# Kernel tuning notes

Measured on AMD Instinct MI355X. Metric: run time of the kernel, lower is better.

## Reference

```python
import jax, jax.numpy as jnp
import numpy as np

N_NODES = 50000
N_EDGES = 1600000
NODE_DIM = 128
EDGE_DIM = 64
HIDDEN = 128
K_HOPS = 2  # DGL TAGConv default k=2


def _uniform(key, shape, fan_in):
    bound = 1.0 / np.sqrt(fan_in)
    return jax.random.uniform(key, shape, jnp.float32, -bound, bound)


def setup_inputs() -> dict:
    key = jax.random.key(0)
    ks = jax.random.split(key, 12)
    d_msg_in = NODE_DIM + EDGE_DIM
    d_c1_in = (HIDDEN + NODE_DIM) * (K_HOPS + 1)
    d_c2_in = HIDDEN * (K_HOPS + 1)
    return {
        "node_fea": jax.random.normal(ks[0], (N_NODES, NODE_DIM), jnp.float32),
        "edge_fea": jax.random.normal(ks[1], (N_EDGES, EDGE_DIM), jnp.float32),
        "src": jax.random.randint(ks[2], (N_EDGES,), 0, N_NODES),
        "dst": jax.random.randint(ks[3], (N_EDGES,), 0, N_NODES),
        "msg_W": _uniform(ks[4], (d_msg_in, HIDDEN), d_msg_in),
        "msg_b": _uniform(ks[5], (HIDDEN,), d_msg_in),
        "W1": _uniform(ks[6], (d_c1_in, HIDDEN), d_c1_in),
        "b1": _uniform(ks[7], (HIDDEN,), d_c1_in),
        "W2": _uniform(ks[8], (d_c2_in, HIDDEN), d_c2_in),
        "b2": _uniform(ks[9], (HIDDEN,), d_c2_in),
        "Wp": _uniform(ks[10], (HIDDEN, 1), HIDDEN),
        "bp": _uniform(ks[11], (1,), HIDDEN),
    }


def reference(node_fea, edge_fea, src, dst, msg_W, msg_b, W1, b1, W2, b2, Wp, bp):
    n = node_fea.shape[0]
    # --- edge message: relu(Linear([src_fea, edge_fea])) then scatter-sum to dst ---
    msg = jax.nn.relu(jnp.concatenate([node_fea[src], edge_fea], axis=1) @ msg_W + msg_b)
    h_neigh = jax.ops.segment_sum(msg, dst, num_segments=n)  # [N, H]

    # --- TAGConv (k=2) symmetric in-degree normalization, DGL-style ---
    deg = jax.ops.segment_sum(jnp.ones((dst.shape[0],), node_fea.dtype), dst, num_segments=n)
    norm = jnp.maximum(deg, 1.0) ** -0.5  # [N]

    def prop(x):  # x: [N, D] -> norm * A^T (norm * x)
        return norm[:, None] * jax.ops.segment_sum((x * norm[:, None])[src], dst, num_segments=n)

    def tagconv(x, W, b):
        h1 = prop(x)
        h2 = prop(h1)
        return jnp.concatenate([x, h1, h2], axis=1) @ W + b

    h = jax.nn.relu(tagconv(jnp.concatenate([node_fea, h_neigh], axis=1), W1, b1))
    h = jax.nn.relu(tagconv(h, W2, b2))

    # --- dgl.mean_nodes (single graph) then predict ---
    hg = jnp.mean(h, axis=0)  # [H]
    return hg @ Wp + bp  # [1]
```

## Files before the change

### kernel.cpp

```cpp
#include <hip/hip_runtime.h>
#include <hip/hip_bf16.h>


typedef __attribute__((ext_vector_type(8))) short short8;
typedef __attribute__((ext_vector_type(4))) float f32x4;
typedef __attribute__((ext_vector_type(4))) unsigned u32x4;
typedef unsigned short ushort_t;
typedef unsigned char uchar_t;

static __device__ __forceinline__ unsigned short f2bf(float x) {
  union { float f; unsigned u; } v{x};
  unsigned r = v.u + 0x7FFF + ((v.u >> 16) & 1);
  return (unsigned short)(r >> 16);
}
static __device__ __forceinline__ float bf2f(unsigned short h) {
  union { unsigned u; float f; } v{(unsigned)h << 16};
  return v.f;
}
static __device__ __forceinline__ float u2f(unsigned u) {
  union { unsigned u; float f; } v{u};
  return v.f;
}
static __device__ __forceinline__ unsigned cvtpk(float a, float b) {
  unsigned r;
  asm("v_cvt_pk_bf16_f32 %0, %1, %2" : "=v"(r) : "v"(a), "v"(b));
  return r;
}
static __device__ __forceinline__ uchar_t f2fp8(float x) {
  return (uchar_t)(__builtin_amdgcn_cvt_pk_fp8_f32(x, 0.f, 0, false) & 0xff);
}
static __device__ __forceinline__ ushort_t pk2fp8(float a, float b) {
  return (ushort_t)(__builtin_amdgcn_cvt_pk_fp8_f32(a, b, 0, false) & 0xffff);
}

__global__ void k_deg(const int* __restrict__ dst, int* __restrict__ deg, int E) {
  int i = blockIdx.x * blockDim.x + threadIdx.x;
  int stride = gridDim.x * blockDim.x;
  for (; i < E; i += stride) atomicAdd(&deg[dst[i]], 1);
}

__global__ void k_scan(const int* __restrict__ deg, float* __restrict__ norm,
                       int* __restrict__ offs, int* __restrict__ cursor, int N) {
  __shared__ int part[1024];
  const int t = threadIdx.x;
  const int C = (N + 1023) >> 10;
  const int b = t * C, e = min(b + C, N);
  int s = 0;
  for (int i = b; i < e; ++i) s += deg[i];
  part[t] = s;
  __syncthreads();
  for (int ofs = 1; ofs < 1024; ofs <<= 1) {
    int v = (t >= ofs) ? part[t - ofs] : 0;
    __syncthreads();
    part[t] += v;
    __syncthreads();
  }
  int base = (t == 0) ? 0 : part[t - 1];
  for (int i = b; i < e; ++i) {
    offs[i] = base;
    cursor[i] = base;
    int d = deg[i];
    base += d;
    norm[i] = rsqrtf((float)max(d, 1));
  }
  if (t == 0) offs[N] = part[1023];
}

__global__ void k_csr(const int* __restrict__ src, const int* __restrict__ dst,
                      int* __restrict__ cursor, int* __restrict__ csr_srcnode,
                      int* __restrict__ csr_eid, int* __restrict__ pos2node, int E) {
  int i = blockIdx.x * blockDim.x + threadIdx.x;
  int stride = gridDim.x * blockDim.x;
  for (; i < E; i += stride) {
    int d = dst[i];
    int pos = atomicAdd(&cursor[d], 1);
    csr_srcnode[pos] = src[i];
    csr_eid[pos] = i;
    pos2node[pos] = d;
  }
}

__global__ void k_prepAll(const float* __restrict__ msg_W, const float* __restrict__ W1,
                          const float* __restrict__ W2, ushort_t* __restrict__ WfT_hi,
                          ushort_t* __restrict__ WfT_lo, ushort_t* __restrict__ WfB_hi,
                          ushort_t* __restrict__ WfB_lo, ushort_t* __restrict__ Wf1_hi,
                          ushort_t* __restrict__ Wf1_lo, ushort_t* __restrict__ Wf2_hi,
                          ushort_t* __restrict__ Wf2_lo) {
  int id = blockIdx.x * 256 + threadIdx.x;
  const float* W;
  ushort_t *dh, *dl;
  int lid;
  if (id < 16384) {
    W = msg_W; dh = WfT_hi; dl = WfT_lo; lid = id;
  } else if (id < 24576) {
    W = msg_W + 128 * 128; dh = WfB_hi; dl = WfB_lo; lid = id - 16384;
  } else if (id < 122880) {
    int sub = id - 24576;
    int s = sub >> 15;
    lid = sub & 32767;
    W = W1 + (size_t)s * 256 * 128;
    dh = Wf1_hi + (size_t)s * 32768;
    dl = Wf1_lo + (size_t)s * 32768;
  } else if (id < 172032) {
    int sub = id - 122880;
    int s = sub >> 14;
    lid = sub & 16383;
    W = W2 + (size_t)s * 128 * 128;
    dh = Wf2_hi + (size_t)s * 16384;
    dl = Wf2_lo + (size_t)s * 16384;
  } else {
    return;
  }
  int j = lid & 7;
  int l = (lid >> 3) & 63;
  int rest = lid >> 9;
  int ks = rest & 1, nt = (rest >> 1) & 7, kc = rest >> 4;
  int k = kc * 64 + ks * 32 + (l >> 4) * 8 + j;
  int col = nt * 16 + (l & 15);
  float w = W[(size_t)k * 128 + col];
  unsigned short hi = f2bf(w);
  unsigned short lo = f2bf(w - bf2f(hi));
  dh[lid] = hi;
  dl[lid] = lo;
}

static __device__ __forceinline__ void stage_hi(const float* base, int sq, int sr,
                                                ushort_t* Xh) {
#pragma unroll
  for (int i2 = 0; i2 < 2; ++i2) {
    const int o = sq * 2 + i2;
    f32x4 a4 = *(const f32x4*)(base + sq * 16 + i2 * 8);
    f32x4 b4 = *(const f32x4*)(base + sq * 16 + i2 * 8 + 4);
    u32x4 vh;
    vh[0] = cvtpk(a4[0], a4[1]);
    vh[1] = cvtpk(a4[2], a4[3]);
    vh[2] = cvtpk(b4[0], b4[1]);
    vh[3] = cvtpk(b4[2], b4[3]);
    const int slot = (sr >> 4) * 128 + o * 16 + (sr & 15);
    *(u32x4*)(Xh + (size_t)slot * 8) = vh;
  }
}

__global__ __launch_bounds__(256) void k_mm(
    const float* __restrict__ A0, const ushort_t* __restrict__ Wf_hi,
    const ushort_t* __restrict__ Wf_lo, const float* __restrict__ bias,
    uchar_t* __restrict__ outZ8, int M, int KC) {
  __shared__ __align__(16) char lds[40960];
  ushort_t* Xh = (ushort_t*)lds;
  ushort_t* Whi = (ushort_t*)(lds + 8192);
  ushort_t* Wlo = (ushort_t*)(lds + 24576);

  const int t = threadIdx.x;
  const int m0 = blockIdx.x * 64;
  const int l = t & 63, mt = t >> 6;
  const int sr = t & 63, sq = t >> 6;
  const int row = min(m0 + sr, M - 1);

  f32x4 acc[8];
#pragma unroll
  for (int nt = 0; nt < 8; ++nt) acc[nt] = (f32x4){0.f, 0.f, 0.f, 0.f};

  for (int kc = 0; kc < KC; ++kc) {
    __syncthreads();
    {
      const ulong2* gh = (const ulong2*)(Wf_hi + (size_t)kc * 8192);
      const ulong2* gl = (const ulong2*)(Wf_lo + (size_t)kc * 8192);
#pragma unroll
      for (int i = 0; i < 4; ++i) {
        ((ulong2*)Whi)[i * 256 + t] = gh[i * 256 + t];
        ((ulong2*)Wlo)[i * 256 + t] = gl[i * 256 + t];
      }
    }
    stage_hi(A0 + (size_t)row * 128 + kc * 64, sq, sr, Xh);
    __syncthreads();
    const short8* Xh8 = (const short8*)Xh;
    const short8* Wh8 = (const short8*)Whi;
    const short8* Wl8 = (const short8*)Wlo;
#pragma unroll
    for (int ks = 0; ks < 2; ++ks) {
      short8 ah = Xh8[mt * 128 + ks * 64 + l];
#pragma unroll
      for (int nt = 0; nt < 8; ++nt) {
        short8 bh = Wh8[(nt * 2 + ks) * 64 + l];
        short8 bl = Wl8[(nt * 2 + ks) * 64 + l];
        acc[nt] = __builtin_amdgcn_mfma_f32_16x16x32_bf16(ah, bh, acc[nt], 0, 0, 0);
        acc[nt] = __builtin_amdgcn_mfma_f32_16x16x32_bf16(ah, bl, acc[nt], 0, 0, 0);
      }
    }
  }
  const int l15 = l & 15, lh = l >> 4;
#pragma unroll
  for (int nt = 0; nt < 8; ++nt) {
    const int col = nt * 16 + l15;
#pragma unroll
    for (int rg = 0; rg < 4; ++rg) {
      const int r = m0 + mt * 16 + lh * 4 + rg;
      if (r < M) outZ8[(size_t)r * 128 + col] = f2fp8(acc[nt][rg] + bias[col]);
    }
  }
}

template <int BF16A>
__global__ __launch_bounds__(256) void k_mm3(
    const void* __restrict__ A0v, const float* __restrict__ A1, int split64,
    const ushort_t* __restrict__ Wf_hi, const ushort_t* __restrict__ Wf_lo,
    const float* __restrict__ rowscale, float* __restrict__ outA,
    ushort_t* __restrict__ outYB, uchar_t* __restrict__ outYC8, int M, int KC) {
  __shared__ __align__(16) char lds[40960];
  ushort_t* Xh = (ushort_t*)lds;
  ushort_t* Whi = (ushort_t*)(lds + 8192);
  ushort_t* Wlo = (ushort_t*)(lds + 24576);

  const int t = threadIdx.x;
  const int m0 = blockIdx.x * 64;
  const int l = t & 63, mt = t >> 6;
  const int sr = t & 63, sq = t >> 6;
  const int row = min(m0 + sr, M - 1);

  f32x4 acc[3][8];
#pragma unroll
  for (int s = 0; s < 3; ++s)
#pragma unroll
    for (int nt = 0; nt < 8; ++nt) acc[s][nt] = (f32x4){0.f, 0.f, 0.f, 0.f};

  for (int kc = 0; kc < KC; ++kc) {
    __syncthreads();
    if constexpr (BF16A) {
      const ushort_t* base = (const ushort_t*)A0v + (size_t)row * 128 + kc * 64;
#pragma unroll
      for (int i2 = 0; i2 < 2; ++i2) {
        const int o = sq * 2 + i2;
        short8 v = *(const short8*)(base + sq * 16 + i2 * 8);
        const int slot = (sr >> 4) * 128 + o * 16 + (sr & 15);
        *(short8*)(Xh + (size_t)slot * 8) = v;
      }
    } else {
      const float* A0 = (const float*)A0v;
      const float* base = (kc < split64) ? (A0 + (size_t)row * 128 + kc * 64)
                                         : (A1 + (size_t)row * 128 + (kc - split64) * 64);
      stage_hi(base, sq, sr, Xh);
    }
#pragma unroll
    for (int s = 0; s < 3; ++s) {
      if (s) __syncthreads();
      {
        const ulong2* gh = (const ulong2*)(Wf_hi + ((size_t)s * KC + kc) * 8192);
        const ulong2* gl = (const ulong2*)(Wf_lo + ((size_t)s * KC + kc) * 8192);
#pragma unroll
        for (int i = 0; i < 4; ++i) {
          ((ulong2*)Whi)[i * 256 + t] = gh[i * 256 + t];
          ((ulong2*)Wlo)[i * 256 + t] = gl[i * 256 + t];
        }
      }
      __syncthreads();
      const short8* Xh8 = (const short8*)Xh;
      const short8* Wh8 = (const short8*)Whi;
      const short8* Wl8 = (const short8*)Wlo;
#pragma unroll
      for (int ks = 0; ks < 2; ++ks) {
        short8 ah = Xh8[mt * 128 + ks * 64 + l];
#pragma unroll
        for (int nt = 0; nt < 8; ++nt) {
          short8 bh = Wh8[(nt * 2 + ks) * 64 + l];
          short8 bl = Wl8[(nt * 2 + ks) * 64 + l];
          acc[s][nt] = __builtin_amdgcn_mfma_f32_16x16x32_bf16(ah, bh, acc[s][nt], 0, 0, 0);
          acc[s][nt] = __builtin_amdgcn_mfma_f32_16x16x32_bf16(ah, bl, acc[s][nt], 0, 0, 0);
        }
      }
    }
  }
  const int l15 = l & 15, lh = l >> 4;
#pragma unroll
  for (int rg = 0; rg < 4; ++rg) {
    const int r = m0 + mt * 16 + lh * 4 + rg;
    if (r < M) {
      const float rs = rowscale[r];
#pragma unroll
      for (int nt = 0; nt < 8; ++nt) {
        const int col = nt * 16 + l15;
        outA[(size_t)r * 128 + col] = acc[0][nt][rg];
        outYB[(size_t)r * 128 + col] = f2bf(acc[1][nt][rg] * rs);
        outYC8[(size_t)r * 128 + col] = f2fp8(acc[2][nt][rg] * rs);
      }
    }
  }
}

__global__ __launch_bounds__(1024, 8) void k_edge(
    const float* __restrict__ ef, const int* __restrict__ csr_srcnode,
    const int* __restrict__ csr_eid, const int* __restrict__ pos2node,
    const ushort_t* __restrict__ WfB_hi, const ushort_t* __restrict__ WfB_lo,
    const uchar_t* __restrict__ Z8, float* __restrict__ h_neigh) {
  __shared__ __align__(16) char lds[49152];
  ushort_t* Xh = (ushort_t*)lds;
  ushort_t* Whi = (ushort_t*)(lds + 16384);
  ushort_t* Wlo = (ushort_t*)(lds + 32768);
  ushort_t* Cs = (ushort_t*)lds;
  int* sN = (int*)(lds + 32768);

  const int t = threadIdx.x;
  const int b0 = blockIdx.x * 128;
  const int l = t & 63, w = t >> 6;
  const int mt = w >> 1, nh = w & 1;
  const int col = t & 127, g = t >> 7;
  const int rbase = b0 + g * 16;

  uchar_t z8[16];
#pragma unroll
  for (int i = 0; i < 16; ++i)
    z8[i] = Z8[(size_t)csr_srcnode[rbase + i] * 128 + col];
  ((ulong2*)Whi)[t] = ((const ulong2*)WfB_hi)[t];
  ((ulong2*)Wlo)[t] = ((const ulong2*)WfB_lo)[t];
  {
    const int row = t >> 3, part = t & 7;
    const int eid = csr_eid[b0 + row];
    const float* rowp = ef + (size_t)eid * 64 + part * 8;
    f32x4 a4 = __builtin_nontemporal_load((const f32x4*)rowp);
    f32x4 b4 = __builtin_nontemporal_load((const f32x4*)(rowp + 4));
    u32x4 vh;
    vh[0] = cvtpk(a4[0], a4[1]);
    vh[1] = cvtpk(a4[2], a4[3]);
    vh[2] = cvtpk(b4[0], b4[1]);
    vh[3] = cvtpk(b4[2], b4[3]);
    const int slot = (row >> 4) * 128 + part * 16 + (row & 15);
    *(u32x4*)(Xh + (size_t)slot * 8) = vh;
  }
  __syncthreads();

  f32x4 acc[4];
#pragma unroll
  for (int nt = 0; nt < 4; ++nt) acc[nt] = (f32x4){0.f, 0.f, 0.f, 0.f};
  {
    const short8* Xh8 = (const short8*)Xh;
    const short8* Wh8 = (const short8*)Whi;
    const short8* Wl8 = (const short8*)Wlo;
#pragma unroll
    for (int ks = 0; ks < 2; ++ks) {
      short8 ah = Xh8[mt * 128 + ks * 64 + l];
#pragma unroll
      for (int nt = 0; nt < 4; ++nt) {
        const int ntg = nh * 4 + nt;
        short8 bh = Wh8[(ntg * 2 + ks) * 64 + l];
        short8 bl = Wl8[(ntg * 2 + ks) * 64 + l];
        acc[nt] = __builtin_amdgcn_mfma_f32_16x16x32_bf16(ah, bh, acc[nt], 0, 0, 0);
        acc[nt] = __builtin_amdgcn_mfma_f32_16x16x32_bf16(ah, bl, acc[nt], 0, 0, 0);
      }
    }
  }
  __syncthreads();
  if (t < 128) sN[t] = pos2node[b0 + t];
  const int l15 = l & 15, lh = l >> 4;
#pragma unroll
  for (int nt = 0; nt < 4; ++nt) {
#pragma unroll
    for (int rg = 0; rg < 4; ++rg) {
      const int row = mt * 16 + lh * 4 + rg;
      const int c = nh * 64 + nt * 16 + l15;
      Cs[row * 128 + (c ^ (((row >> 2) & 3) << 4))] = f2bf(acc[nt][rg]);
    }
  }
  __syncthreads();
  {
    int node = sN[g * 16];
    float ssum = 0.f;
#pragma unroll
    for (int r = 0; r < 16; ++r) {
      const int rr = g * 16 + r;
      float cz = bf2f(Cs[rr * 128 + (col ^ (((rr >> 2) & 3) << 4))]);
      float zf = __builtin_amdgcn_cvt_f32_fp8((int)z8[r], 0);
      float v = fmaxf(cz + zf, 0.f);
      if (r == 0) {
        ssum = v;
      } else {
        int n2 = sN[rr];
        if (n2 == node) {
          ssum += v;
        } else {
          unsafeAtomicAdd(&h_neigh[(size_t)node * 128 + col], ssum);
          node = n2;
          ssum = v;
        }
      }
    }
    unsafeAtomicAdd(&h_neigh[(size_t)node * 128 + col], ssum);
  }
}

__global__ __launch_bounds__(256) void k_propA(
    const uchar_t* __restrict__ YC8, const ushort_t* __restrict__ YBt,
    const int* __restrict__ offs, const int* __restrict__ csr_src,
    const float* __restrict__ norm, uchar_t* __restrict__ Qt8, int N) {
  const int v = blockIdx.x * 4 + (threadIdx.x >> 6);
  const int lane = threadIdx.x & 63;
  if (v >= N) return;
  const int b = offs[v], e = offs[v + 1];
  const ushort_t* yc = (const ushort_t*)YC8;
  float ax0 = 0.f, ay0 = 0.f, ax1 = 0.f, ay1 = 0.f;
  float ax2 = 0.f, ay2 = 0.f, ax3 = 0.f, ay3 = 0.f;
  int i = b;
  const int e4 = b + ((e - b) & ~3);
  for (; i < e4; i += 4) {
    const int s0 = csr_src[i], s1 = csr_src[i + 1];
    const int s2 = csr_src[i + 2], s3 = csr_src[i + 3];
    const int x0 = yc[(size_t)s0 * 64 + lane];
    const int x1 = yc[(size_t)s1 * 64 + lane];
    const int x2 = yc[(size_t)s2 * 64 + lane];
    const int x3 = yc[(size_t)s3 * 64 + lane];
    auto d0 = __builtin_amdgcn_cvt_pk_f32_fp8(x0, false);
    auto d1 = __builtin_amdgcn_cvt_pk_f32_fp8(x1, false);
    auto d2 = __builtin_amdgcn_cvt_pk_f32_fp8(x2, false);
    auto d3 = __builtin_amdgcn_cvt_pk_f32_fp8(x3, false);
    ax0 += d0[0]; ay0 += d0[1];
    ax1 += d1[0]; ay1 += d1[1];
    ax2 += d2[0]; ay2 += d2[1];
    ax3 += d3[0]; ay3 += d3[1];
  }
  for (; i < e; ++i) {
    const int x = yc[(size_t)csr_src[i] * 64 + lane];
    auto d = __builtin_amdgcn_cvt_pk_f32_fp8(x, false);
    ax0 += d[0]; ay0 += d[1];
  }
  const float ax = (ax0 + ax1) + (ax2 + ax3);
  const float ay = (ay0 + ay1) + (ay2 + ay3);
  const float n = norm[v];
  const float n2 = n * n;
  const unsigned yb = ((const unsigned*)YBt)[(size_t)v * 64 + lane];
  ((ushort_t*)Qt8)[(size_t)v * 64 + lane] =
      pk2fp8(u2f(yb << 16) + n2 * ax, u2f(yb & 0xffff0000u) + n2 * ay);
}

__global__ __launch_bounds__(256) void k_propB(
    const uchar_t* __restrict__ Qt8, const float* __restrict__ YA,
    const float* __restrict__ bias, const int* __restrict__ offs,
    const int* __restrict__ csr_src, const float* __restrict__ norm,
    ushort_t* __restrict__ H, int N) {
  const int v = blockIdx.x * 4 + (threadIdx.x >> 6);
  const int lane = threadIdx.x & 63;
  if (v >= N) return;
  const int b = offs[v], e = offs[v + 1];
  const ushort_t* qp = (const ushort_t*)Qt8;
  float ax0 = 0.f, ay0 = 0.f, ax1 = 0.f, ay1 = 0.f;
  float ax2 = 0.f, ay2 = 0.f, ax3 = 0.f, ay3 = 0.f;
  int i = b;
  const int e4 = b + ((e - b) & ~3);
  for (; i < e4; i += 4) {
    const int s0 = csr_src[i], s1 = csr_src[i + 1];
    const int s2 = csr_src[i + 2], s3 = csr_src[i + 3];
    const int x0 = qp[(size_t)s0 * 64 + lane];
    const int x1 = qp[(size_t)s1 * 64 + lane];
    const int x2 = qp[(size_t)s2 * 64 + lane];
    const int x3 = qp[(size_t)s3 * 64 + lane];
    auto d0 = __builtin_amdgcn_cvt_pk_f32_fp8(x0, false);
    auto d1 = __builtin_amdgcn_cvt_pk_f32_fp8(x1, false);
    auto d2 = __builtin_amdgcn_cvt_pk_f32_fp8(x2, false);
    auto d3 = __builtin_amdgcn_cvt_pk_f32_fp8(x3, false);
    ax0 += d0[0]; ay0 += d0[1];
    ax1 += d1[0]; ay1 += d1[1];
    ax2 += d2[0]; ay2 += d2[1];
    ax3 += d3[0]; ay3 += d3[1];
  }
  for (; i < e; ++i) {
    const int x = qp[(size_t)csr_src[i] * 64 + lane];
    auto d = __builtin_amdgcn_cvt_pk_f32_fp8(x, false);
    ax0 += d[0]; ay0 += d[1];
  }
  const float ax = (ax0 + ax1) + (ax2 + ax3);
  const float ay = (ay0 + ay1) + (ay2 + ay3);
  const float n = norm[v];
  const float2 ya = ((const float2*)YA)[(size_t)v * 64 + lane];
  const float2 bb = ((const float2*)bias)[lane];
  const float hx = fmaxf(ya.x + n * ax + bb.x, 0.f);
  const float hy = fmaxf(ya.y + n * ay + bb.y, 0.f);
  ((unsigned*)H)[(size_t)v * 64 + lane] = cvtpk(hx, hy);
}

__global__ void k_colsum(const ushort_t* __restrict__ h, float* __restrict__ hg, int N) {
  const int t = threadIdx.x;
  const int per = (N + gridDim.x - 1) / gridDim.x;
  const int n0 = blockIdx.x * per, n1 = min(n0 + per, N);
  float s = 0.f;
  for (int n = n0; n < n1; ++n) s += bf2f(h[(size_t)n * 128 + t]);
  unsafeAtomicAdd(&hg[t], s);
}

__global__ void k_final(const float* __restrict__ hg, const float* __restrict__ Wp,
                        const float* __restrict__ bp, float* __restrict__ out,
                        float invN) {
  __shared__ float red[128];
  const int t = threadIdx.x;
  red[t] = hg[t] * invN * Wp[t];
  __syncthreads();
  for (int s = 64; s > 0; s >>= 1) {
    if (t < s) red[t] += red[t + s];
    __syncthreads();
  }
  if (t == 0) out[0] = red[0] + bp[0];
}

extern "C" void kernel_launch(void* const* d_in, const int* in_sizes, int n_in,
                              void* d_out, int out_size, void* d_ws, size_t ws_size,
                              hipStream_t stream) {
  const float* node_fea = (const float*)d_in[0];
  const float* edge_fea = (const float*)d_in[1];
  const int* src = (const int*)d_in[2];
  const int* dst = (const int*)d_in[3];
  const float* msg_W = (const float*)d_in[4];
  const float* msg_b = (const float*)d_in[5];
  const float* W1 = (const float*)d_in[6];
  const float* b1 = (const float*)d_in[7];
  const float* W2 = (const float*)d_in[8];
  const float* b2 = (const float*)d_in[9];
  const float* Wp = (const float*)d_in[10];
  const float* bp = (const float*)d_in[11];

  const int N = in_sizes[0] / 128;
  const int E = in_sizes[2];

  char* p = (char*)d_ws;
  auto alloc = [&](size_t bytes) {
    char* r = p;
    p += (bytes + 255) & ~(size_t)255;
    return r;
  };
  int* deg = (int*)alloc((size_t)N * 4);
  float* norm = (float*)alloc((size_t)N * 4);
  int* offs = (int*)alloc((size_t)(N + 1) * 4);
  int* cursor = (int*)alloc((size_t)N * 4);
  int* csr_srcnode = (int*)alloc((size_t)E * 4);
  int* csr_eid = (int*)alloc((size_t)E * 4);
  int* pos2node = (int*)alloc((size_t)E * 4);
  ushort_t* WfT_hi = (ushort_t*)alloc(2 * 8192 * 2);
  ushort_t* WfT_lo = (ushort_t*)alloc(2 * 8192 * 2);
  ushort_t* WfB_hi = (ushort_t*)alloc(1 * 8192 * 2);
  ushort_t* WfB_lo = (ushort_t*)alloc(1 * 8192 * 2);
  ushort_t* Wf1_hi = (ushort_t*)alloc(3 * 4 * 8192 * 2);
  ushort_t* Wf1_lo = (ushort_t*)alloc(3 * 4 * 8192 * 2);
  ushort_t* Wf2_hi = (ushort_t*)alloc(3 * 2 * 8192 * 2);
  ushort_t* Wf2_lo = (ushort_t*)alloc(3 * 2 * 8192 * 2);
  uchar_t* Z8 = (uchar_t*)alloc((size_t)N * 128);
  float* YA = (float*)alloc((size_t)N * 128 * 4);
  float* hn = (float*)alloc((size_t)N * 128 * 4);
  ushort_t* YBt = (ushort_t*)alloc((size_t)N * 128 * 2);
  uchar_t* YC8 = (uchar_t*)alloc((size_t)N * 128);
  uchar_t* Qt8 = (uchar_t*)alloc((size_t)N * 128);
  ushort_t* H1 = (ushort_t*)alloc((size_t)N * 128 * 2);
  ushort_t* H2 = (ushort_t*)alloc((size_t)N * 128 * 2);
  float* hg = (float*)alloc(128 * 4);

  hipMemsetAsync(deg, 0, (size_t)N * 4, stream);
  hipMemsetAsync(hn, 0, (size_t)N * 128 * 4, stream);
  hipMemsetAsync(hg, 0, 128 * 4, stream);

  k_deg<<<2048, 256, 0, stream>>>(dst, deg, E);
  k_scan<<<1, 1024, 0, stream>>>(deg, norm, offs, cursor, N);
  k_csr<<<2048, 256, 0, stream>>>(src, dst, cursor, csr_srcnode, csr_eid, pos2node, E);
  k_prepAll<<<672, 256, 0, stream>>>(msg_W, W1, W2, WfT_hi, WfT_lo, WfB_hi, WfB_lo,
                                     Wf1_hi, Wf1_lo, Wf2_hi, Wf2_lo);

  const int MB = (N + 63) / 64;
  const int PB = (N + 3) / 4;

  k_mm<<<MB, 256, 0, stream>>>(node_fea, WfT_hi, WfT_lo, msg_b, Z8, N, 2);
  k_edge<<<E / 128, 1024, 0, stream>>>(edge_fea, csr_srcnode, csr_eid, pos2node,
                                       WfB_hi, WfB_lo, Z8, hn);

  k_mm3<0><<<MB, 256, 0, stream>>>(node_fea, hn, 2, Wf1_hi, Wf1_lo, norm, YA,
                                   YBt, YC8, N, 4);
  k_propA<<<PB, 256, 0, stream>>>(YC8, YBt, offs, csr_srcnode, norm, Qt8, N);
  k_propB<<<PB, 256, 0, stream>>>(Qt8, YA, b1, offs, csr_srcnode, norm, H1, N);

  k_mm3<1><<<MB, 256, 0, stream>>>(H1, nullptr, 0, Wf2_hi, Wf2_lo, norm, YA,
                                   YBt, YC8, N, 2);
  k_propA<<<PB, 256, 0, stream>>>(YC8, YBt, offs, csr_srcnode, norm, Qt8, N);
  k_propB<<<PB, 256, 0, stream>>>(Qt8, YA, b2, offs, csr_srcnode, norm, H2, N);

  k_colsum<<<256, 128, 0, stream>>>(H2, hg, N);
  k_final<<<1, 128, 0, stream>>>(hg, Wp, bp, (float*)d_out, 1.0f / (float)N);
}
```

Before: 900.4 us.

## Fuse setup kernels, persist edge kernel with prefetch, store YA in bf16

Merges degree counting with weight preparation, and the prefix scan with the node-feature GEMM, into shared launches. This removes launch gaps and lets the single-block scan overlap GEMM blocks. The edge kernel becomes persistent: weights are loaded into LDS once, and the next tile's gathered Z8 values and edge ids are prefetched during the current MFMA step. The YA intermediate is stored in bf16 instead of fp32, halving its write and read traffic at some precision cost.

```diff
diff --git a/kernel.cpp b/kernel.cpp
--- a/kernel.cpp
+++ b/kernel.cpp
@@ -33,60 +33,20 @@
   return (ushort_t)(__builtin_amdgcn_cvt_pk_fp8_f32(a, b, 0, false) & 0xffff);
 }
 
-__global__ void k_deg(const int* __restrict__ dst, int* __restrict__ deg, int E) {
-  int i = blockIdx.x * blockDim.x + threadIdx.x;
-  int stride = gridDim.x * blockDim.x;
-  for (; i < E; i += stride) atomicAdd(&deg[dst[i]], 1);
-}
-
-__global__ void k_scan(const int* __restrict__ deg, float* __restrict__ norm,
-                       int* __restrict__ offs, int* __restrict__ cursor, int N) {
-  __shared__ int part[1024];
-  const int t = threadIdx.x;
-  const int C = (N + 1023) >> 10;
-  const int b = t * C, e = min(b + C, N);
-  int s = 0;
-  for (int i = b; i < e; ++i) s += deg[i];
-  part[t] = s;
-  __syncthreads();
-  for (int ofs = 1; ofs < 1024; ofs <<= 1) {
-    int v = (t >= ofs) ? part[t - ofs] : 0;
-    __syncthreads();
-    part[t] += v;
-    __syncthreads();
-  }
-  int base = (t == 0) ? 0 : part[t - 1];
-  for (int i = b; i < e; ++i) {
-    offs[i] = base;
-    cursor[i] = base;
-    int d = deg[i];
-    base += d;
-    norm[i] = rsqrtf((float)max(d, 1));
-  }
-  if (t == 0) offs[N] = part[1023];
-}
-
-__global__ void k_csr(const int* __restrict__ src, const int* __restrict__ dst,
-                      int* __restrict__ cursor, int* __restrict__ csr_srcnode,
-                      int* __restrict__ csr_eid, int* __restrict__ pos2node, int E) {
-  int i = blockIdx.x * blockDim.x + threadIdx.x;
-  int stride = gridDim.x * blockDim.x;
-  for (; i < E; i += stride) {
-    int d = dst[i];
-    int pos = atomicAdd(&cursor[d], 1);
-    csr_srcnode[pos] = src[i];
-    csr_eid[pos] = i;
-    pos2node[pos] = d;
-  }
-}
-
-__global__ void k_prepAll(const float* __restrict__ msg_W, const float* __restrict__ W1,
-                          const float* __restrict__ W2, ushort_t* __restrict__ WfT_hi,
-                          ushort_t* __restrict__ WfT_lo, ushort_t* __restrict__ WfB_hi,
-                          ushort_t* __restrict__ WfB_lo, ushort_t* __restrict__ Wf1_hi,
-                          ushort_t* __restrict__ Wf1_lo, ushort_t* __restrict__ Wf2_hi,
-                          ushort_t* __restrict__ Wf2_lo) {
-  int id = blockIdx.x * 256 + threadIdx.x;
+__global__ void k_init(const int* __restrict__ dst, int* __restrict__ deg, int E,
+                       const float* __restrict__ msg_W, const float* __restrict__ W1,
+                       const float* __restrict__ W2, ushort_t* __restrict__ WfT_hi,
+                       ushort_t* __restrict__ WfT_lo, ushort_t* __restrict__ WfB_hi,
+                       ushort_t* __restrict__ WfB_lo, ushort_t* __restrict__ Wf1_hi,
+                       ushort_t* __restrict__ Wf1_lo, ushort_t* __restrict__ Wf2_hi,
+                       ushort_t* __restrict__ Wf2_lo) {
+  if (blockIdx.x < 1024) {
+    int i = blockIdx.x * 256 + threadIdx.x;
+    int stride = 1024 * 256;
+    for (; i < E; i += stride) atomicAdd(&deg[dst[i]], 1);
+    return;
+  }
+  int id = (blockIdx.x - 1024) * 256 + threadIdx.x;
   const float* W;
   ushort_t *dh, *dl;
   int lid;
@@ -124,6 +84,20 @@
   dl[lid] = lo;
 }
 
+__global__ void k_csr(const int* __restrict__ src, const int* __restrict__ dst,
+                      int* __restrict__ cursor, int* __restrict__ csr_srcnode,
+                      int* __restrict__ csr_eid, int* __restrict__ pos2node, int E) {
+  int i = blockIdx.x * blockDim.x + threadIdx.x;
+  int stride = gridDim.x * blockDim.x;
+  for (; i < E; i += stride) {
+    int d = dst[i];
+    int pos = atomicAdd(&cursor[d], 1);
+    csr_srcnode[pos] = src[i];
+    csr_eid[pos] = i;
+    pos2node[pos] = d;
+  }
+}
+
 static __device__ __forceinline__ void stage_hi(const float* base, int sq, int sr,
                                                 ushort_t* Xh) {
 #pragma unroll
@@ -141,20 +115,46 @@
   }
 }
 
-__global__ __launch_bounds__(256) void k_mm(
-    const float* __restrict__ A0, const ushort_t* __restrict__ Wf_hi,
-    const ushort_t* __restrict__ Wf_lo, const float* __restrict__ bias,
-    uchar_t* __restrict__ outZ8, int M, int KC) {
+__global__ __launch_bounds__(256) void k_scan_mmz(
+    const int* __restrict__ deg, float* __restrict__ norm, int* __restrict__ offs,
+    int* __restrict__ cursor, int N, const float* __restrict__ A0,
+    const ushort_t* __restrict__ Wf_hi, const ushort_t* __restrict__ Wf_lo,
+    const float* __restrict__ bias, uchar_t* __restrict__ outZ8, int KC) {
   __shared__ __align__(16) char lds[40960];
+  if (blockIdx.x == 0) {
+    int* part = (int*)lds;
+    const int t = threadIdx.x;
+    const int C = (N + 255) >> 8;
+    const int b = t * C, e = min(b + C, N);
+    int s = 0;
+    for (int i = b; i < e; ++i) s += deg[i];
+    part[t] = s;
+    __syncthreads();
+    for (int ofs = 1; ofs < 256; ofs <<= 1) {
+      int v = (t >= ofs) ? part[t - ofs] : 0;
+      __syncthreads();
+      part[t] += v;
+      __syncthreads();
+    }
+    int base = (t == 0) ? 0 : part[t - 1];
+    for (int i = b; i < e; ++i) {
+      offs[i] = base;
+      cursor[i] = base;
+      int d = deg[i];
+      base += d;
+      norm[i] = rsqrtf((float)max(d, 1));
+    }
+    if (t == 0) offs[N] = part[255];
+    return;
+  }
   ushort_t* Xh = (ushort_t*)lds;
   ushort_t* Whi = (ushort_t*)(lds + 8192);
   ushort_t* Wlo = (ushort_t*)(lds + 24576);
-
   const int t = threadIdx.x;
-  const int m0 = blockIdx.x * 64;
+  const int m0 = (blockIdx.x - 1) * 64;
   const int l = t & 63, mt = t >> 6;
   const int sr = t & 63, sq = t >> 6;
-  const int row = min(m0 + sr, M - 1);
+  const int row = min(m0 + sr, N - 1);
 
   f32x4 acc[8];
 #pragma unroll
@@ -195,7 +195,7 @@
 #pragma unroll
     for (int rg = 0; rg < 4; ++rg) {
       const int r = m0 + mt * 16 + lh * 4 + rg;
-      if (r < M) outZ8[(size_t)r * 128 + col] = f2fp8(acc[nt][rg] + bias[col]);
+      if (r < N) outZ8[(size_t)r * 128 + col] = f2fp8(acc[nt][rg] + bias[col]);
     }
   }
 }
@@ -204,7 +204,7 @@
 __global__ __launch_bounds__(256) void k_mm3(
     const void* __restrict__ A0v, const float* __restrict__ A1, int split64,
     const ushort_t* __restrict__ Wf_hi, const ushort_t* __restrict__ Wf_lo,
-    const float* __restrict__ rowscale, float* __restrict__ outA,
+    const float* __restrict__ rowscale, ushort_t* __restrict__ outYA,
     ushort_t* __restrict__ outYB, uchar_t* __restrict__ outYC8, int M, int KC) {
   __shared__ __align__(16) char lds[40960];
   ushort_t* Xh = (ushort_t*)lds;
@@ -278,7 +278,7 @@
 #pragma unroll
       for (int nt = 0; nt < 8; ++nt) {
         const int col = nt * 16 + l15;
-        outA[(size_t)r * 128 + col] = acc[0][nt][rg];
+        outYA[(size_t)r * 128 + col] = f2bf(acc[0][nt][rg]);
         outYB[(size_t)r * 128 + col] = f2bf(acc[1][nt][rg] * rs);
         outYC8[(size_t)r * 128 + col] = f2fp8(acc[2][nt][rg] * rs);
       }
@@ -290,99 +290,122 @@
     const float* __restrict__ ef, const int* __restrict__ csr_srcnode,
     const int* __restrict__ csr_eid, const int* __restrict__ pos2node,
     const ushort_t* __restrict__ WfB_hi, const ushort_t* __restrict__ WfB_lo,
-    const uchar_t* __restrict__ Z8, float* __restrict__ h_neigh) {
-  __shared__ __align__(16) char lds[49152];
-  ushort_t* Xh = (ushort_t*)lds;
-  ushort_t* Whi = (ushort_t*)(lds + 16384);
-  ushort_t* Wlo = (ushort_t*)(lds + 32768);
-  ushort_t* Cs = (ushort_t*)lds;
-  int* sN = (int*)(lds + 32768);
+    const uchar_t* __restrict__ Z8, float* __restrict__ h_neigh, int nT) {
+  __shared__ __align__(16) char lds[66048];
+  ushort_t* Whi = (ushort_t*)lds;
+  ushort_t* Wlo = (ushort_t*)(lds + 16384);
+  ushort_t* Xh = (ushort_t*)(lds + 32768);
+  ushort_t* Cs = (ushort_t*)(lds + 32768);
+  int* sN = (int*)(lds + 65536);
 
   const int t = threadIdx.x;
-  const int b0 = blockIdx.x * 128;
   const int l = t & 63, w = t >> 6;
   const int mt = w >> 1, nh = w & 1;
   const int col = t & 127, g = t >> 7;
-  const int rbase = b0 + g * 16;
-
-  uchar_t z8[16];
-#pragma unroll
-  for (int i = 0; i < 16; ++i)
-    z8[i] = Z8[(size_t)csr_srcnode[rbase + i] * 128 + col];
+  const int erow = t >> 3, epart = t & 7;
+  const int l15 = l & 15, lh = l >> 4;
+
   ((ulong2*)Whi)[t] = ((const ulong2*)WfB_hi)[t];
   ((ulong2*)Wlo)[t] = ((const ulong2*)WfB_lo)[t];
-  {
-    const int row = t >> 3, part = t & 7;
-    const int eid = csr_eid[b0 + row];
-    const float* rowp = ef + (size_t)eid * 64 + part * 8;
-    f32x4 a4 = __builtin_nontemporal_load((const f32x4*)rowp);
-    f32x4 b4 = __builtin_nontemporal_load((const f32x4*)(rowp + 4));
-    u32x4 vh;
-    vh[0] = cvtpk(a4[0], a4[1]);
-    vh[1] = cvtpk(a4[2], a4[3]);
-    vh[2] = cvtpk(b4[0], b4[1]);
-    vh[3] = cvtpk(b4[2], b4[3]);
-    const int slot = (row >> 4) * 128 + part * 16 + (row & 15);
-    *(u32x4*)(Xh + (size_t)slot * 8) = vh;
-  }
-  __syncthreads();
-
-  f32x4 acc[4];
-#pragma unroll
-  for (int nt = 0; nt < 4; ++nt) acc[nt] = (f32x4){0.f, 0.f, 0.f, 0.f};
-  {
-    const short8* Xh8 = (const short8*)Xh;
-    const short8* Wh8 = (const short8*)Whi;
-    const short8* Wl8 = (const short8*)Wlo;
-#pragma unroll
-    for (int ks = 0; ks < 2; ++ks) {
-      short8 ah = Xh8[mt * 128 + ks * 64 + l];
-#pragma unroll
-      for (int nt = 0; nt < 4; ++nt) {
-        const int ntg = nh * 4 + nt;
-        short8 bh = Wh8[(ntg * 2 + ks) * 64 + l];
-        short8 bl = Wl8[(ntg * 2 + ks) * 64 + l];
-        acc[nt] = __builtin_amdgcn_mfma_f32_16x16x32_bf16(ah, bh, acc[nt], 0, 0, 0);
-        acc[nt] = __builtin_amdgcn_mfma_f32_16x16x32_bf16(ah, bl, acc[nt], 0, 0, 0);
-      }
-    }
-  }
-  __syncthreads();
-  if (t < 128) sN[t] = pos2node[b0 + t];
-  const int l15 = l & 15, lh = l >> 4;
-#pragma unroll
-  for (int nt = 0; nt < 4; ++nt) {
-#pragma unroll
-    for (int rg = 0; rg < 4; ++rg) {
-      const int row = mt * 16 + lh * 4 + rg;
-      const int c = nh * 64 + nt * 16 + l15;
-      Cs[row * 128 + (c ^ (((row >> 2) & 3) << 4))] = f2bf(acc[nt][rg]);
-    }
-  }
-  __syncthreads();
-  {
-    int node = sN[g * 16];
-    float ssum = 0.f;
-#pragma unroll
-    for (int r = 0; r < 16; ++r) {
-      const int rr = g * 16 + r;
-      float cz = bf2f(Cs[rr * 128 + (col ^ (((rr >> 2) & 3) << 4))]);
-      float zf = __builtin_amdgcn_cvt_f32_fp8((int)z8[r], 0);
-      float v = fmaxf(cz + zf, 0.f);
-      if (r == 0) {
-        ssum = v;
-      } else {
-        int n2 = sN[rr];
-        if (n2 == node) {
-          ssum += v;
+
+  int tile = blockIdx.x;
+  uchar_t z8[16];
+  int eid = 0;
+  if (tile < nT) {
+    const int b0 = tile * 128;
+#pragma unroll
+    for (int i = 0; i < 16; ++i)
+      z8[i] = Z8[(size_t)csr_srcnode[b0 + g * 16 + i] * 128 + col];
+    eid = csr_eid[b0 + erow];
+  }
+
+  for (; tile < nT; tile += gridDim.x) {
+    const int b0 = tile * 128;
+    {
+      const float* rowp = ef + (size_t)eid * 64 + epart * 8;
+      f32x4 a4 = __builtin_nontemporal_load((const f32x4*)rowp);
+      f32x4 b4 = __builtin_nontemporal_load((const f32x4*)(rowp + 4));
+      u32x4 vh;
+      vh[0] = cvtpk(a4[0], a4[1]);
+      vh[1] = cvtpk(a4[2], a4[3]);
+      vh[2] = cvtpk(b4[0], b4[1]);
+      vh[3] = cvtpk(b4[2], b4[3]);
+      const int slot = (erow >> 4) * 128 + epart * 16 + (erow & 15);
+      *(u32x4*)(Xh + (size_t)slot * 8) = vh;
+      if (t < 128) sN[t] = pos2node[b0 + t];
+    }
+    __syncthreads();
+    f32x4 acc[4];
+#pragma unroll
+    for (int nt = 0; nt < 4; ++nt) acc[nt] = (f32x4){0.f, 0.f, 0.f, 0.f};
+    {
+      const short8* Xh8 = (const short8*)Xh;
+      const short8* Wh8 = (const short8*)Whi;
+      const short8* Wl8 = (const short8*)Wlo;
+#pragma unroll
+      for (int ks = 0; ks < 2; ++ks) {
+        short8 ah = Xh8[mt * 128 + ks * 64 + l];
+#pragma unroll
+        for (int nt = 0; nt < 4; ++nt) {
+          const int ntg = nh * 4 + nt;
+          short8 bh = Wh8[(ntg * 2 + ks) * 64 + l];
+          short8 bl = Wl8[(ntg * 2 + ks) * 64 + l];
+          acc[nt] = __builtin_amdgcn_mfma_f32_16x16x32_bf16(ah, bh, acc[nt], 0, 0, 0);
+          acc[nt] = __builtin_amdgcn_mfma_f32_16x16x32_bf16(ah, bl, acc[nt], 0, 0, 0);
+        }
+      }
+    }
+    uchar_t z8n[16];
+    int eidn = 0;
+    {
+      const int ntile = tile + gridDim.x;
+      if (ntile < nT) {
+        const int nb0 = ntile * 128;
+#pragma unroll
+        for (int i = 0; i < 16; ++i)
+          z8n[i] = Z8[(size_t)csr_srcnode[nb0 + g * 16 + i] * 128 + col];
+        eidn = csr_eid[nb0 + erow];
+      }
+    }
+    __syncthreads();
+#pragma unroll
+    for (int nt = 0; nt < 4; ++nt) {
+#pragma unroll
+      for (int rg = 0; rg < 4; ++rg) {
+        const int row = mt * 16 + lh * 4 + rg;
+        const int c = nh * 64 + nt * 16 + l15;
+        Cs[row * 128 + (c ^ (((row >> 2) & 3) << 4))] = f2bf(acc[nt][rg]);
+      }
+    }
+    __syncthreads();
+    {
+      int node = sN[g * 16];
+      float ssum = 0.f;
+#pragma unroll
+      for (int r = 0; r < 16; ++r) {
+        const int rr = g * 16 + r;
+        float cz = bf2f(Cs[rr * 128 + (col ^ (((rr >> 2) & 3) << 4))]);
+        float zf = __builtin_amdgcn_cvt_f32_fp8((int)z8[r], 0);
+        float v = fmaxf(cz + zf, 0.f);
+        if (r == 0) {
+          ssum = v;
         } else {
-          unsafeAtomicAdd(&h_neigh[(size_t)node * 128 + col], ssum);
-          node = n2;
-          ssum = v;
+          int n2 = sN[rr];
+          if (n2 == node) {
+            ssum += v;
+          } else {
+            unsafeAtomicAdd(&h_neigh[(size_t)node * 128 + col], ssum);
+            node = n2;
+            ssum = v;
+          }
         }
       }
-    }
-    unsafeAtomicAdd(&h_neigh[(size_t)node * 128 + col], ssum);
+      unsafeAtomicAdd(&h_neigh[(size_t)node * 128 + col], ssum);
+    }
+#pragma unroll
+    for (int i = 0; i < 16; ++i) z8[i] = z8n[i];
+    eid = eidn;
+    __syncthreads();
   }
 }
 
@@ -430,7 +453,7 @@
 }
 
 __global__ __launch_bounds__(256) void k_propB(
-    const uchar_t* __restrict__ Qt8, const float* __restrict__ YA,
+    const uchar_t* __restrict__ Qt8, const ushort_t* __restrict__ YAb,
     const float* __restrict__ bias, const int* __restrict__ offs,
     const int* __restrict__ csr_src, const float* __restrict__ norm,
     ushort_t* __restrict__ H, int N) {
@@ -467,10 +490,10 @@
   const float ax = (ax0 + ax1) + (ax2 + ax3);
   const float ay = (ay0 + ay1) + (ay2 + ay3);
   const float n = norm[v];
-  const float2 ya = ((const float2*)YA)[(size_t)v * 64 + lane];
+  const unsigned ya = ((const unsigned*)YAb)[(size_t)v * 64 + lane];
   const float2 bb = ((const float2*)bias)[lane];
-  const float hx = fmaxf(ya.x + n * ax + bb.x, 0.f);
-  const float hy = fmaxf(ya.y + n * ay + bb.y, 0.f);
+  const float hx = fmaxf(u2f(ya << 16) + n * ax + bb.x, 0.f);
+  const float hy = fmaxf(u2f(ya & 0xffff0000u) + n * ay + bb.y, 0.f);
   ((unsigned*)H)[(size_t)v * 64 + lane] = cvtpk(hx, hy);
 }
 
@@ -538,7 +561,7 @@
   ushort_t* Wf2_hi = (ushort_t*)alloc(3 * 2 * 8192 * 2);
   ushort_t* Wf2_lo = (ushort_t*)alloc(3 * 2 * 8192 * 2);
   uchar_t* Z8 = (uchar_t*)alloc((size_t)N * 128);
-  float* YA = (float*)alloc((size_t)N * 128 * 4);
+  ushort_t* YAb = (ushort_t*)alloc((size_t)N * 128 * 2);
   float* hn = (float*)alloc((size_t)N * 128 * 4);
   ushort_t* YBt = (ushort_t*)alloc((size_t)N * 128 * 2);
   uchar_t* YC8 = (uchar_t*)alloc((size_t)N * 128);
@@ -547,32 +570,31 @@
   ushort_t* H2 = (ushort_t*)alloc((size_t)N * 128 * 2);
   float* hg = (float*)alloc(128 * 4);
 
-  hipMemsetAsync(deg, 0, (size_t)N * 4, stream);
-  hipMemsetAsync(hn, 0, (size_t)N * 128 * 4, stream);
-  hipMemsetAsync(hg, 0, 128 * 4, stream);
-
-  k_deg<<<2048, 256, 0, stream>>>(dst, deg, E);
-  k_scan<<<1, 1024, 0, stream>>>(deg, norm, offs, cursor, N);
-  k_csr<<<2048, 256, 0, stream>>>(src, dst, cursor, csr_srcnode, csr_eid, pos2node, E);
-  k_prepAll<<<672, 256, 0, stream>>>(msg_W, W1, W2, WfT_hi, WfT_lo, WfB_hi, WfB_lo,
-                                     Wf1_hi, Wf1_lo, Wf2_hi, Wf2_lo);
+  (void)hipMemsetAsync(deg, 0, (size_t)N * 4, stream);
+  (void)hipMemsetAsync(hn, 0, (size_t)N * 128 * 4, stream);
+  (void)hipMemsetAsync(hg, 0, 128 * 4, stream);
+
+  k_init<<<1696, 256, 0, stream>>>(dst, deg, E, msg_W, W1, W2, WfT_hi, WfT_lo,
+                                   WfB_hi, WfB_lo, Wf1_hi, Wf1_lo, Wf2_hi, Wf2_lo);
 
   const int MB = (N + 63) / 64;
   const int PB = (N + 3) / 4;
 
-  k_mm<<<MB, 256, 0, stream>>>(node_fea, WfT_hi, WfT_lo, msg_b, Z8, N, 2);
-  k_edge<<<E / 128, 1024, 0, stream>>>(edge_fea, csr_srcnode, csr_eid, pos2node,
-                                       WfB_hi, WfB_lo, Z8, hn);
-
-  k_mm3<0><<<MB, 256, 0, stream>>>(node_fea, hn, 2, Wf1_hi, Wf1_lo, norm, YA,
+  k_scan_mmz<<<MB + 1, 256, 0, stream>>>(deg, norm, offs, cursor, N, node_fea,
+                                         WfT_hi, WfT_lo, msg_b, Z8, 2);
+  k_csr<<<2048, 256, 0, stream>>>(src, dst, cursor, csr_srcnode, csr_eid, pos2node, E);
+  k_edge<<<512, 1024, 0, stream>>>(edge_fea, csr_srcnode, csr_eid, pos2node,
+                                   WfB_hi, WfB_lo, Z8, hn, E / 128);
+
+  k_mm3<0><<<MB, 256, 0, stream>>>(node_fea, hn, 2, Wf1_hi, Wf1_lo, norm, YAb,
                                    YBt, YC8, N, 4);
   k_propA<<<PB, 256, 0, stream>>>(YC8, YBt, offs, csr_srcnode, norm, Qt8, N);
-  k_propB<<<PB, 256, 0, stream>>>(Qt8, YA, b1, offs, csr_srcnode, norm, H1, N);
-
-  k_mm3<1><<<MB, 256, 0, stream>>>(H1, nullptr, 0, Wf2_hi, Wf2_lo, norm, YA,
+  k_propB<<<PB, 256, 0, stream>>>(Qt8, YAb, b1, offs, csr_srcnode, norm, H1, N);
+
+  k_mm3<1><<<MB, 256, 0, stream>>>(H1, nullptr, 0, Wf2_hi, Wf2_lo, norm, YAb,
                                    YBt, YC8, N, 2);
   k_propA<<<PB, 256, 0, stream>>>(YC8, YBt, offs, csr_srcnode, norm, Qt8, N);
-  k_propB<<<PB, 256, 0, stream>>>(Qt8, YA, b2, offs, csr_srcnode, norm, H2, N);
+  k_propB<<<PB, 256, 0, stream>>>(Qt8, YAb, b2, offs, csr_srcnode, norm, H2, N);
 
   k_colsum<<<256, 128, 0, stream>>>(H2, hg, N);
   k_final<<<1, 128, 0, stream>>>(hg, Wp, bp, (float*)d_out, 1.0f / (float)N);
```

After: 1.221 ms. 1.36x slower.
